# Kernel tuning notes

Hardware: AMD Instinct MI355X
Metric: run time of the kernel (lower is better)

## Reference

```python
import jax, jax.numpy as jnp
import numpy as np

NH = 8        # num_heads
HD = 6        # head_dim
DIM = NH * HD # 48
KS = 3        # kernel_size
NT = KS ** 3  # 27 neighborhood tokens
SCALE = HD ** -0.5


def setup_inputs() -> dict:
    key = jax.random.key(0)
    k1, k2, k3 = jax.random.split(key, 3)
    B, H, W, T = 1, 40, 40, 40
    q = jax.random.normal(k1, (B, H, W, T, DIM), jnp.float32)
    k = jax.random.normal(k2, (B, H, W, T, DIM), jnp.float32)
    # learned relative position bias (torch init is zeros; use small noise so it matters)
    rpb = jax.random.normal(k3, (NH, KS, KS, KS), jnp.float32) * 0.02
    return {"q": q, "k": k, "rpb": rpb}


def _neighborhood_attention(q, k, rpb):
    B, H, W, T, C = q.shape
    # pad keys by win_size=1 on each spatial side (zero pad, as in nnf.pad)
    kp = jnp.pad(k, ((0, 0), (1, 1), (1, 1), (1, 1), (0, 0)))
    # gather the 27 shifted views -> [B,H,W,T,27,C] (equivalent of unfold+permute)
    win = jnp.stack(
        [kp[:, i:i + H, j:j + W, l:l + T, :]
         for i in range(KS) for j in range(KS) for l in range(KS)],
        axis=4,
    )
    qh = q.reshape(B, H, W, T, NH, HD) * SCALE          # [B,H,W,T,nh,hd]
    kh = win.reshape(B, H, W, T, NT, NH, HD)            # [B,H,W,T,27,nh,hd]
    attn = jnp.einsum('bxyzhd,bxyzkhd->bxyzhk', qh, kh)
    attn = attn + rpb.reshape(NH, NT)[None, None, None, None]  # rel-pos bias
    attn = jax.nn.softmax(attn, axis=-1)                # [B,H,W,T,nh,27]
    # value = constant integer offsets of the 3x3x3 window (makeV)
    r = jnp.arange(-(KS // 2), KS // 2 + 1, dtype=q.dtype)
    offs = jnp.stack(jnp.meshgrid(r, r, r, indexing='ij'), axis=-1).reshape(NT, 3)
    out = jnp.einsum('bxyzhk,ko->bxyzho', attn, offs)   # [B,H,W,T,nh,3]
    return out.reshape(B, H, W, T, NH * 3).transpose(0, 4, 1, 2, 3)


def reference(q, k, rpb):
    return _neighborhood_attention(q, k, rpb)
```

## Files before the change

### kernel.cpp

```cpp
#include <hip/hip_runtime.h>


#define GS    40
#define NVOX  (GS*GS*GS)
#define S4ST  872
#define S2ST  440
#define S2OFF (4*S4ST)

typedef __fp16 half2_t __attribute__((ext_vector_type(2)));
typedef float  f2      __attribute__((ext_vector_type(2)));

__device__ __forceinline__ float fdot2(half2_t a, half2_t b, float c) {
    return __builtin_amdgcn_fdot2(a, b, c, false);
}
__device__ __forceinline__ half2_t h2(unsigned int u) {
    return __builtin_bit_cast(half2_t, u);
}

__global__ __launch_bounds__(256) void natt_kernel(
    const float* __restrict__ q, const float* __restrict__ kk,
    const float* __restrict__ rpb, float* __restrict__ out)
{
    __shared__ __align__(16) unsigned int sk[4 * S4ST + 4 * S2ST];
    __shared__ float srpb[4 * 27 * 2];

    int t = threadIdx.x;
    int b = blockIdx.x;
    int w = (b & 7) * 125 + (b >> 3);
    int bz = w % 10, by = (w / 10) % 10, bx = w / 100;
    int x0 = bx * 4, y0 = by * 4, z0 = bz * 4;

    int hp = t & 3;
    int v  = t >> 2;
    int vz = v & 3, vy = (v >> 2) & 3, vx = v >> 4;
    int gvox = (x0 + vx) * 1600 + (y0 + vy) * 40 + (z0 + vz);
    const float4* qp = (const float4*)q + (size_t)gvox * 12 + hp * 3;
    float4 qa = qp[0], qb = qp[1], qc = qp[2];

    if (t < 216) {
        int h = t / 27, n = t % 27;
        srpb[((h >> 1) * 27 + n) * 2 + (h & 1)] = rpb[t] * 1.4426950408889634f;
    }

    const float4* kk4 = (const float4*)kk;
    #pragma unroll
    for (int it = 0; it < 11; ++it) {
        int idx = t + it * 256;
        if (idx < 2592) {
            int row = idx / 72;
            int off = idx - row * 72;
            int zz  = off / 12;
            int g   = off - zz * 12;
            int xi = row / 6, yi = row - xi * 6;
            int gx = x0 + xi - 1, gy = y0 + yi - 1, gz = z0 + zz - 1;
            float4 val = make_float4(0.f, 0.f, 0.f, 0.f);
            if (((unsigned)gx < GS) & ((unsigned)gy < GS) & ((unsigned)gz < GS))
                val = kk4[(gx * 1600 + gy * 40 + gz) * 12 + g];
            int hp_c = g / 3, cc = g - hp_c * 3;
            int hvv  = row * 6 + zz;
            uint2 u;
            u.x = __builtin_bit_cast(unsigned int,
                    __builtin_amdgcn_cvt_pkrtz(val.x, val.y));
            u.y = __builtin_bit_cast(unsigned int,
                    __builtin_amdgcn_cvt_pkrtz(val.z, val.w));
            unsigned int* dst = (cc == 2)
                ? sk + S2OFF + hp_c * S2ST + hvv * 2
                : sk + hp_c * S4ST + hvv * 4 + cc * 2;
            *(uint2*)dst = u;
        }
    }

    const float QS = 0.4082482904638631f * 1.4426950408889634f;
    half2_t qh0 = __builtin_amdgcn_cvt_pkrtz(qa.x * QS, qa.y * QS);
    half2_t qh1 = __builtin_amdgcn_cvt_pkrtz(qa.z * QS, qa.w * QS);
    half2_t qh2 = __builtin_amdgcn_cvt_pkrtz(qb.x * QS, qb.y * QS);
    half2_t qh3 = __builtin_amdgcn_cvt_pkrtz(qb.z * QS, qb.w * QS);
    half2_t qh4 = __builtin_amdgcn_cvt_pkrtz(qc.x * QS, qc.y * QS);
    half2_t qh5 = __builtin_amdgcn_cvt_pkrtz(qc.z * QS, qc.w * QS);

    __syncthreads();

    const uint4* k4p = (const uint4*)sk + hp * (S4ST / 4);
    const uint2* k2p = (const uint2*)(sk + S2OFF) + hp * (S2ST / 2);
    const f2*    rp2 = (const f2*)srpb + hp * 27;

    f2 den = {0, 0}, ozc = {0, 0};
    f2 xp = {0, 0}, xm = {0, 0}, yp = {0, 0}, ym = {0, 0};

    #pragma unroll
    for (int i = 0; i < 3; ++i)
    #pragma unroll
    for (int j = 0; j < 3; ++j) {
        int hv0 = (vx + i) * 36 + (vy + j) * 6 + vz;
        f2 ev[3];
        #pragma unroll
        for (int l = 0; l < 3; ++l) {
            uint4 a = k4p[hv0 + l];
            uint2 c = k2p[hv0 + l];
            f2 rp = rp2[i * 9 + j * 3 + l];
            float d0 = fdot2(qh0, h2(a.x),
                       fdot2(qh1, h2(a.y),
                       fdot2(qh2, h2(a.z), rp.x)));
            float d1 = fdot2(qh3, h2(a.w),
                       fdot2(qh4, h2(c.x),
                       fdot2(qh5, h2(c.y), rp.y)));
            f2 e;
            e.x = __builtin_amdgcn_exp2f(d0);
            e.y = __builtin_amdgcn_exp2f(d1);
            ev[l] = e;
        }
        f2 A = ev[0] + ev[1] + ev[2];
        den += A;
        ozc += ev[2] - ev[0];
        if (i == 0)      xm += A;
        else if (i == 2) xp += A;
        if (j == 0)      ym += A;
        else if (j == 2) yp += A;
    }

    f2 oxv = xp - xm, oyv = yp - ym;
    float inv0 = __builtin_amdgcn_rcpf(den.x);
    float inv1 = __builtin_amdgcn_rcpf(den.y);

    float* op = out + (size_t)(hp * 6) * NVOX + gvox;
    op[0*NVOX] = oxv.x * inv0;
    op[1*NVOX] = oyv.x * inv0;
    op[2*NVOX] = ozc.x * inv0;
    op[3*NVOX] = oxv.y * inv1;
    op[4*NVOX] = oyv.y * inv1;
    op[5*NVOX] = ozc.y * inv1;
}

extern "C" void kernel_launch(void* const* d_in, const int* in_sizes, int n_in,
                              void* d_out, int out_size, void* d_ws, size_t ws_size,
                              hipStream_t stream) {
    const float* q   = (const float*)d_in[0];
    const float* k   = (const float*)d_in[1];
    const float* rpb = (const float*)d_in[2];
    float* out = (float*)d_out;

    natt_kernel<<<1000, 256, 0, stream>>>(q, k, rpb, out);
}
```

Before: 15.18 us.

## Restructure key staging with per-voxel table and voxel-major shared layout

Precomputes a per-halo-voxel table of clamped global offsets plus a validity bit, then stages keys with 8 threads per voxel. Each thread does two float4 loads and one 16-byte shared store, replacing the divide-heavy per-float4 index math and branching. Shared memory becomes voxel-major with a 36-word stride, and the rpb bias is repacked so it can be read with vector loads. This adds an extra barrier, and the new stride may change LDS bank conflicts in the compute loop.

```diff
diff --git a/kernel.cpp b/kernel.cpp
--- a/kernel.cpp
+++ b/kernel.cpp
@@ -1,11 +1,9 @@
 #include <hip/hip_runtime.h>
 
 
-#define GS    40
-#define NVOX  (GS*GS*GS)
-#define S4ST  872
-#define S2ST  440
-#define S2OFF (4*S4ST)
+#define GS   40
+#define NVOX (GS*GS*GS)
+#define VST  36
 
 typedef __fp16 half2_t __attribute__((ext_vector_type(2)));
 typedef float  f2      __attribute__((ext_vector_type(2)));
@@ -16,13 +14,17 @@
 __device__ __forceinline__ half2_t h2(unsigned int u) {
     return __builtin_bit_cast(half2_t, u);
 }
+__device__ __forceinline__ unsigned int pk(float a, float b) {
+    return __builtin_bit_cast(unsigned int, __builtin_amdgcn_cvt_pkrtz(a, b));
+}
 
 __global__ __launch_bounds__(256) void natt_kernel(
     const float* __restrict__ q, const float* __restrict__ kk,
     const float* __restrict__ rpb, float* __restrict__ out)
 {
-    __shared__ __align__(16) unsigned int sk[4 * S4ST + 4 * S2ST];
-    __shared__ float srpb[4 * 27 * 2];
+    __shared__ __align__(16) unsigned int sk[224 * VST];
+    __shared__ float srpb[4 * 72];
+    __shared__ int   vtab[224];
 
     int t = threadIdx.x;
     int b = blockIdx.x;
@@ -37,77 +39,87 @@
     const float4* qp = (const float4*)q + (size_t)gvox * 12 + hp * 3;
     float4 qa = qp[0], qb = qp[1], qc = qp[2];
 
+    if (t < 224) {
+        int vvc = t < 216 ? t : 215;
+        int xi = vvc / 36, r36 = vvc - xi * 36;
+        int yi = r36 / 6,  zi  = r36 - yi * 6;
+        int gx = x0 + xi - 1, gy = y0 + yi - 1, gz = z0 + zi - 1;
+        bool val = (((unsigned)gx < GS) & ((unsigned)gy < GS) &
+                    ((unsigned)gz < GS)) && (t < 216);
+        int cx = min(max(gx, 0), GS - 1);
+        int cy = min(max(gy, 0), GS - 1);
+        int cz = min(max(gz, 0), GS - 1);
+        vtab[t] = ((cx * 1600 + cy * 40 + cz) * 12) | (val ? (1 << 30) : 0);
+    }
     if (t < 216) {
-        int h = t / 27, n = t % 27;
-        srpb[((h >> 1) * 27 + n) * 2 + (h & 1)] = rpb[t] * 1.4426950408889634f;
+        int h = t / 27, n = t - h * 27;
+        int i = n / 9, r9 = n - i * 9;
+        int j = r9 / 3, l = r9 - j * 3;
+        srpb[(h >> 1) * 72 + ((i * 3 + j) * 4 + l) * 2 + (h & 1)] =
+            rpb[t] * 1.4426950408889634f;
     }
+    __syncthreads();
 
-    const float4* kk4 = (const float4*)kk;
-    #pragma unroll
-    for (int it = 0; it < 11; ++it) {
-        int idx = t + it * 256;
-        if (idx < 2592) {
-            int row = idx / 72;
-            int off = idx - row * 72;
-            int zz  = off / 12;
-            int g   = off - zz * 12;
-            int xi = row / 6, yi = row - xi * 6;
-            int gx = x0 + xi - 1, gy = y0 + yi - 1, gz = z0 + zz - 1;
-            float4 val = make_float4(0.f, 0.f, 0.f, 0.f);
-            if (((unsigned)gx < GS) & ((unsigned)gy < GS) & ((unsigned)gz < GS))
-                val = kk4[(gx * 1600 + gy * 40 + gz) * 12 + g];
-            int hp_c = g / 3, cc = g - hp_c * 3;
-            int hvv  = row * 6 + zz;
-            uint2 u;
-            u.x = __builtin_bit_cast(unsigned int,
-                    __builtin_amdgcn_cvt_pkrtz(val.x, val.y));
-            u.y = __builtin_bit_cast(unsigned int,
-                    __builtin_amdgcn_cvt_pkrtz(val.z, val.w));
-            unsigned int* dst = (cc == 2)
-                ? sk + S2OFF + hp_c * S2ST + hvv * 2
-                : sk + hp_c * S4ST + hvv * 4 + cc * 2;
-            *(uint2*)dst = u;
+    {
+        const float4* kk4 = (const float4*)kk;
+        int sub = t & 7;
+        int hpc = sub >> 1, pt = sub & 1;
+        int soffA = hpc * 3 + pt * 2;
+        int soffB = soffA + (pt ? 0 : 1);
+        unsigned int* dstb = sk + (t >> 3) * VST + hpc * 8 + pt * 4;
+        const int* vtp = vtab + (t >> 3);
+        #pragma unroll
+        for (int it = 0; it < 7; ++it) {
+            int rec = vtp[it * 32];
+            unsigned m = (unsigned)(((int)(rec << 1)) >> 31);
+            int base = rec & 0x3FFFFFFF;
+            float4 fA = kk4[base + soffA];
+            float4 fB = kk4[base + soffB];
+            uint4 u;
+            u.x = pk(fA.x, fA.y) & m; u.y = pk(fA.z, fA.w) & m;
+            u.z = pk(fB.x, fB.y) & m; u.w = pk(fB.z, fB.w) & m;
+            *(uint4*)(dstb + it * 32 * VST) = u;
         }
     }
 
     const float QS = 0.4082482904638631f * 1.4426950408889634f;
-    half2_t qh0 = __builtin_amdgcn_cvt_pkrtz(qa.x * QS, qa.y * QS);
-    half2_t qh1 = __builtin_amdgcn_cvt_pkrtz(qa.z * QS, qa.w * QS);
-    half2_t qh2 = __builtin_amdgcn_cvt_pkrtz(qb.x * QS, qb.y * QS);
-    half2_t qh3 = __builtin_amdgcn_cvt_pkrtz(qb.z * QS, qb.w * QS);
-    half2_t qh4 = __builtin_amdgcn_cvt_pkrtz(qc.x * QS, qc.y * QS);
-    half2_t qh5 = __builtin_amdgcn_cvt_pkrtz(qc.z * QS, qc.w * QS);
+    half2_t qh0 = __builtin_amdgcn_cvt_pkrtz(qa.x*QS, qa.y*QS);
+    half2_t qh1 = __builtin_amdgcn_cvt_pkrtz(qa.z*QS, qa.w*QS);
+    half2_t qh2 = __builtin_amdgcn_cvt_pkrtz(qb.x*QS, qb.y*QS);
+    half2_t qh3 = __builtin_amdgcn_cvt_pkrtz(qb.z*QS, qb.w*QS);
+    half2_t qh4 = __builtin_amdgcn_cvt_pkrtz(qc.x*QS, qc.y*QS);
+    half2_t qh5 = __builtin_amdgcn_cvt_pkrtz(qc.z*QS, qc.w*QS);
 
     __syncthreads();
 
-    const uint4* k4p = (const uint4*)sk + hp * (S4ST / 4);
-    const uint2* k2p = (const uint2*)(sk + S2OFF) + hp * (S2ST / 2);
-    const f2*    rp2 = (const f2*)srpb + hp * 27;
+    const unsigned int* kbp = sk + (vx * 36 + vy * 6 + vz) * VST + hp * 8;
+    const float* rbp = srpb + hp * 72;
 
-    f2 den = {0, 0}, ozc = {0, 0};
-    f2 xp = {0, 0}, xm = {0, 0}, yp = {0, 0}, ym = {0, 0};
+    f2 den = {0,0}, ozc = {0,0};
+    f2 xp = {0,0}, xm = {0,0}, yp = {0,0}, ym = {0,0};
 
     #pragma unroll
     for (int i = 0; i < 3; ++i)
     #pragma unroll
     for (int j = 0; j < 3; ++j) {
-        int hv0 = (vx + i) * 36 + (vy + j) * 6 + vz;
+        const unsigned int* cb = kbp + (i * 36 + j * 6) * VST;
+        float4 rp01 = *(const float4*)(rbp + (i * 3 + j) * 8);
+        f2     rp2v = *(const f2*)(rbp + (i * 3 + j) * 8 + 4);
         f2 ev[3];
         #pragma unroll
         for (int l = 0; l < 3; ++l) {
-            uint4 a = k4p[hv0 + l];
-            uint2 c = k2p[hv0 + l];
-            f2 rp = rp2[i * 9 + j * 3 + l];
+            uint4 a = *(const uint4*)(cb + l * VST);
+            uint2 c = *(const uint2*)(cb + l * VST + 4);
+            float rx = (l == 0) ? rp01.x : (l == 1) ? rp01.z : rp2v.x;
+            float ry = (l == 0) ? rp01.y : (l == 1) ? rp01.w : rp2v.y;
             float d0 = fdot2(qh0, h2(a.x),
                        fdot2(qh1, h2(a.y),
-                       fdot2(qh2, h2(a.z), rp.x)));
+                       fdot2(qh2, h2(a.z), rx)));
             float d1 = fdot2(qh3, h2(a.w),
                        fdot2(qh4, h2(c.x),
-                       fdot2(qh5, h2(c.y), rp.y)));
-            f2 e;
-            e.x = __builtin_amdgcn_exp2f(d0);
-            e.y = __builtin_amdgcn_exp2f(d1);
-            ev[l] = e;
+                       fdot2(qh5, h2(c.y), ry)));
+            ev[l].x = __builtin_amdgcn_exp2f(d0);
+            ev[l].y = __builtin_amdgcn_exp2f(d1);
         }
         f2 A = ev[0] + ev[1] + ev[2];
         den += A;
```

After: 14.45 us. 4.8% less time.
